# Kernel tuning notes

Measured on AMD Instinct MI355X. Metric: run time of the kernel, lower is better.

## Reference

```python
import jax, jax.numpy as jnp
import numpy as np

B, A, D, H = 2048, 32, 128, 256

def setup_inputs() -> dict:
    key = jax.random.key(0)
    ks = jax.random.split(key, 12)
    s = lambda fan_in: 1.0 / np.sqrt(fan_in)
    return {
        "obs": jax.random.normal(ks[0], (B, A, D), dtype=jnp.float32),
        "act": jax.random.normal(ks[1], (B, A, 8), dtype=jnp.float32),
        "enc_W": jax.random.uniform(ks[2], (H, D), jnp.float32, -s(D), s(D)),
        "enc_b": jax.random.uniform(ks[3], (H,), jnp.float32, -s(D), s(D)),
        "fobs_W": jax.random.uniform(ks[4], (H, H), jnp.float32, -s(H), s(H)),
        "fobs_b": jax.random.uniform(ks[5], (H,), jnp.float32, -s(H), s(H)),
        "W_ih": jax.random.uniform(ks[6], (3 * H, H), jnp.float32, -s(H), s(H)),
        "b_ih": jax.random.uniform(ks[7], (3 * H,), jnp.float32, -s(H), s(H)),
        "W_hh": jax.random.uniform(ks[8], (3 * H, H), jnp.float32, -s(H), s(H)),
        "b_hh": jax.random.uniform(ks[9], (3 * H,), jnp.float32, -s(H), s(H)),
        "dec_W": jax.random.uniform(ks[10], (1, H), jnp.float32, -s(H), s(H)),
        "dec_b": jax.random.uniform(ks[11], (1,), jnp.float32, -s(H), s(H)),
    }

def _gru_cell(x, h, W_ih, b_ih, W_hh, b_hh):
    # torch.nn.GRUCell: gates stacked as [reset, update, new]
    gi = x @ W_ih.T + b_ih          # [N, 3H]
    gh = h @ W_hh.T + b_hh          # [N, 3H]
    i_r, i_z, i_n = jnp.split(gi, 3, axis=-1)
    h_r, h_z, h_n = jnp.split(gh, 3, axis=-1)
    r = jax.nn.sigmoid(i_r + h_r)
    z = jax.nn.sigmoid(i_z + h_z)
    n = jnp.tanh(i_n + r * h_n)
    return (1.0 - z) * n + z * h

def reference(obs, act, enc_W, enc_b, fobs_W, fobs_b, W_ih, b_ih, W_hh, b_hh, dec_W, dec_b):
    b, a, d = obs.shape
    x = obs.reshape(b * a, d)                         # [B*A, D]
    e = jax.nn.relu(x @ enc_W.T + enc_b)              # encoder + ReLU
    h = e @ fobs_W.T + fobs_b                         # h_out
    # k = 0: comm input is zeros
    h = _gru_cell(jnp.zeros_like(h), h, W_ih, b_ih, W_hh, b_hh)
    # k = 1: masked mean over other agents == (sum_j h_j - h_i) / n_agents
    hA = h.reshape(b, a, -1)                          # [B, A, H]
    c = (hA.sum(axis=1, keepdims=True) - hA) / a      # [B, A, H]
    h = _gru_cell(c.reshape(b * a, -1), h, W_ih, b_ih, W_hh, b_hh)
    return (h @ dec_W.T + dec_b).reshape(b, a, -1)    # [B, A, 1]
```

## Files before the change

### kernel.cpp

```cpp
#include <hip/hip_runtime.h>
#include <hip/hip_fp16.h>


#define NB   2048
#define NA   32
#define DIN  128
#define HID  256
#define SA   264

typedef _Float16 half8  __attribute__((ext_vector_type(8)));
typedef float    float4v __attribute__((ext_vector_type(4)));

#define ENC_OFF    0
#define FOBS_OFF   32768
#define WIH_OFF    98304
#define WHH_OFF    294912
#define PREP_TOTAL 491520

__global__ void prep_weights(const float* __restrict__ encW, const float* __restrict__ fobsW,
                             const float* __restrict__ wih,  const float* __restrict__ whh,
                             _Float16* __restrict__ prep) {
    int F = blockIdx.x * 256 + threadIdx.x;
    if (F >= PREP_TOTAL) return;
    const float* src; int K, NT, local = F;
    if (F < FOBS_OFF)     { src = encW;  K = 128; NT = 16; }
    else if (F < WIH_OFF) { src = fobsW; K = 256; NT = 16; local = F - FOBS_OFF; }
    else if (F < WHH_OFF) { src = wih;   K = 256; NT = 48; local = F - WIH_OFF; }
    else                  { src = whh;   K = 256; NT = 48; local = F - WHH_OFF; }
    int j    = local & 7;
    int lane = (local >> 3) & 63;
    int t    = local >> 9;
    int nt   = t % NT;
    int ks   = t / NT;
    int col  = nt * 16 + (lane & 15);
    int k    = ks * 32 + ((lane >> 4) << 3) + j;
    prep[F] = (_Float16)src[col * K + k];
}

__device__ __forceinline__ float sigmoid_f(float x) {
    x = fminf(fmaxf(x, -30.f), 30.f);
    return 1.f / (1.f + __expf(-x));
}
__device__ __forceinline__ float tanh_f(float x) {
    x = fminf(fmaxf(x, -15.f), 15.f);
    float e = __expf(-2.f * x);
    return (1.f - e) / (1.f + e);
}

__device__ __forceinline__ void zero22(float4v a[2][2]) {
    float4v z = {0.f, 0.f, 0.f, 0.f};
    a[0][0] = z; a[0][1] = z; a[1][0] = z; a[1][1] = z;
}

template<int KSTEPS>
__device__ __forceinline__ void gemm_tile(const _Float16* __restrict__ Abuf,
        const _Float16* __restrict__ prepm, int NT, int ntg0,
        const float* __restrict__ raw, int K, int use_prep,
        int lane, float4v acc[2][2])
{
    const int l16 = lane & 15;
    const int kq  = (lane >> 4) << 3;
    #pragma unroll
    for (int ks = 0; ks < KSTEPS; ks++) {
        int kbase = ks * 32 + kq;
        half8 a0 = *(const half8*)(Abuf + l16 * SA + kbase);
        half8 a1 = *(const half8*)(Abuf + (16 + l16) * SA + kbase);
        half8 b0, b1;
        if (use_prep) {
            b0 = *(const half8*)(prepm + (((ks * NT + ntg0    ) * 64 + lane) << 3));
            b1 = *(const half8*)(prepm + (((ks * NT + ntg0 + 1) * 64 + lane) << 3));
        } else {
            #pragma unroll
            for (int j = 0; j < 8; j++) {
                b0[j] = (_Float16)raw[(ntg0 * 16 + l16) * K + kbase + j];
                b1[j] = (_Float16)raw[((ntg0 + 1) * 16 + l16) * K + kbase + j];
            }
        }
        acc[0][0] = __builtin_amdgcn_mfma_f32_16x16x32_f16(a0, b0, acc[0][0], 0, 0, 0);
        acc[0][1] = __builtin_amdgcn_mfma_f32_16x16x32_f16(a0, b1, acc[0][1], 0, 0, 0);
        acc[1][0] = __builtin_amdgcn_mfma_f32_16x16x32_f16(a1, b0, acc[1][0], 0, 0, 0);
        acc[1][1] = __builtin_amdgcn_mfma_f32_16x16x32_f16(a1, b1, acc[1][1], 0, 0, 0);
    }
}

__global__ __launch_bounds__(512) void commnet_fused(
    const float* __restrict__ obs, const _Float16* __restrict__ prep,
    const float* __restrict__ enc_b, const float* __restrict__ fobs_b,
    const float* __restrict__ b_ih, const float* __restrict__ b_hh,
    const float* __restrict__ dec_W, const float* __restrict__ dec_b,
    float* __restrict__ out,
    const float* __restrict__ encW, const float* __restrict__ fobsW,
    const float* __restrict__ wih, const float* __restrict__ whh,
    int use_prep)
{
    const int b    = blockIdx.x;
    const int tid  = threadIdx.x;
    const int lane = tid & 63;
    const int w    = tid >> 6;
    const int l16  = lane & 15;
    const int quad = lane >> 4;
    const int ntl0 = w * 2;

    __shared__ __align__(16) _Float16 sA[3][NA * SA];
    __shared__ float S[HID];

    const float* obsb = obs + (size_t)b * NA * DIN;
    for (int i = tid; i < NA * DIN; i += 512) {
        int r = i >> 7, k = i & 127;
        sA[0][r * SA + k] = (_Float16)obsb[i];
    }
    if (tid < HID) S[tid] = 0.f;
    __syncthreads();

    float4v acc[2][2];

    zero22(acc);
    gemm_tile<4>(&sA[0][0], prep + ENC_OFF, 16, ntl0, encW, DIN, use_prep, lane, acc);
    #pragma unroll
    for (int nn = 0; nn < 2; nn++) {
        int col = (ntl0 + nn) * 16 + l16;
        float bb = enc_b[col];
        #pragma unroll
        for (int mt = 0; mt < 2; mt++)
            #pragma unroll
            for (int r = 0; r < 4; r++) {
                int row = mt * 16 + quad * 4 + r;
                float v = acc[mt][nn][r] + bb;
                sA[1][row * SA + col] = (_Float16)fmaxf(v, 0.f);
            }
    }
    __syncthreads();

    zero22(acc);
    gemm_tile<8>(&sA[1][0], prep + FOBS_OFF, 16, ntl0, fobsW, HID, use_prep, lane, acc);
    #pragma unroll
    for (int nn = 0; nn < 2; nn++) {
        int col = (ntl0 + nn) * 16 + l16;
        float bb = fobs_b[col];
        #pragma unroll
        for (int mt = 0; mt < 2; mt++)
            #pragma unroll
            for (int r = 0; r < 4; r++) {
                int row = mt * 16 + quad * 4 + r;
                sA[0][row * SA + col] = (_Float16)(acc[mt][nn][r] + bb);
            }
    }
    __syncthreads();

    float rn[2][2][4];
    zero22(acc);
    gemm_tile<8>(&sA[0][0], prep + WHH_OFF, 48, 0 + ntl0, whh, HID, use_prep, lane, acc);
    #pragma unroll
    for (int nn = 0; nn < 2; nn++) {
        int col = (ntl0 + nn) * 16 + l16;
        float bi = b_ih[col], bh = b_hh[col];
        #pragma unroll
        for (int mt = 0; mt < 2; mt++)
            #pragma unroll
            for (int r = 0; r < 4; r++)
                rn[mt][nn][r] = sigmoid_f(bi + acc[mt][nn][r] + bh);
    }
    zero22(acc);
    gemm_tile<8>(&sA[0][0], prep + WHH_OFF, 48, 32 + ntl0, whh, HID, use_prep, lane, acc);
    #pragma unroll
    for (int nn = 0; nn < 2; nn++) {
        int col = (ntl0 + nn) * 16 + l16;
        float bi = b_ih[512 + col], bh = b_hh[512 + col];
        #pragma unroll
        for (int mt = 0; mt < 2; mt++)
            #pragma unroll
            for (int r = 0; r < 4; r++)
                rn[mt][nn][r] = tanh_f(bi + rn[mt][nn][r] * (acc[mt][nn][r] + bh));
    }
    zero22(acc);
    gemm_tile<8>(&sA[0][0], prep + WHH_OFF, 48, 16 + ntl0, whh, HID, use_prep, lane, acc);
    #pragma unroll
    for (int nn = 0; nn < 2; nn++) {
        int col = (ntl0 + nn) * 16 + l16;
        float bi = b_ih[256 + col], bh = b_hh[256 + col];
        float ssum = 0.f;
        #pragma unroll
        for (int mt = 0; mt < 2; mt++)
            #pragma unroll
            for (int r = 0; r < 4; r++) {
                int row = mt * 16 + quad * 4 + r;
                float z = sigmoid_f(bi + acc[mt][nn][r] + bh);
                float hold = (float)sA[0][row * SA + col];
                float h1 = (1.f - z) * rn[mt][nn][r] + z * hold;
                sA[1][row * SA + col] = (_Float16)h1;
                ssum += h1;
            }
        atomicAdd(&S[col], ssum);
    }
    __syncthreads();

    for (int i = tid; i < NA * HID; i += 512) {
        int r = i >> 8, k = i & 255;
        float hv = (float)sA[1][r * SA + k];
        sA[2][r * SA + k] = (_Float16)((S[k] - hv) * (1.f / 32.f));
    }
    __syncthreads();
    if (tid < NA) S[tid] = 0.f;
    __syncthreads();

    float4v acci[2][2], acch[2][2];
    zero22(acci); zero22(acch);
    gemm_tile<8>(&sA[2][0], prep + WIH_OFF, 48, 0 + ntl0, wih, HID, use_prep, lane, acci);
    gemm_tile<8>(&sA[1][0], prep + WHH_OFF, 48, 0 + ntl0, whh, HID, use_prep, lane, acch);
    #pragma unroll
    for (int nn = 0; nn < 2; nn++) {
        int col = (ntl0 + nn) * 16 + l16;
        float bi = b_ih[col], bh = b_hh[col];
        #pragma unroll
        for (int mt = 0; mt < 2; mt++)
            #pragma unroll
            for (int r = 0; r < 4; r++)
                rn[mt][nn][r] = sigmoid_f(acci[mt][nn][r] + bi + acch[mt][nn][r] + bh);
    }
    zero22(acci); zero22(acch);
    gemm_tile<8>(&sA[2][0], prep + WIH_OFF, 48, 32 + ntl0, wih, HID, use_prep, lane, acci);
    gemm_tile<8>(&sA[1][0], prep + WHH_OFF, 48, 32 + ntl0, whh, HID, use_prep, lane, acch);
    #pragma unroll
    for (int nn = 0; nn < 2; nn++) {
        int col = (ntl0 + nn) * 16 + l16;
        float bi = b_ih[512 + col], bh = b_hh[512 + col];
        #pragma unroll
        for (int mt = 0; mt < 2; mt++)
            #pragma unroll
            for (int r = 0; r < 4; r++)
                rn[mt][nn][r] = tanh_f((acci[mt][nn][r] + bi) + rn[mt][nn][r] * (acch[mt][nn][r] + bh));
    }
    zero22(acci); zero22(acch);
    gemm_tile<8>(&sA[2][0], prep + WIH_OFF, 48, 16 + ntl0, wih, HID, use_prep, lane, acci);
    gemm_tile<8>(&sA[1][0], prep + WHH_OFF, 48, 16 + ntl0, whh, HID, use_prep, lane, acch);
    #pragma unroll
    for (int nn = 0; nn < 2; nn++) {
        int col = (ntl0 + nn) * 16 + l16;
        float bi = b_ih[256 + col], bh = b_hh[256 + col];
        #pragma unroll
        for (int mt = 0; mt < 2; mt++)
            #pragma unroll
            for (int r = 0; r < 4; r++) {
                int row = mt * 16 + quad * 4 + r;
                float z = sigmoid_f(acci[mt][nn][r] + bi + acch[mt][nn][r] + bh);
                float h1v = (float)sA[1][row * SA + col];
                rn[mt][nn][r] = (1.f - z) * rn[mt][nn][r] + z * h1v;
            }
    }

    float dw0 = dec_W[(ntl0    ) * 16 + l16];
    float dw1 = dec_W[(ntl0 + 1) * 16 + l16];
    float p[2][4];
    #pragma unroll
    for (int mt = 0; mt < 2; mt++)
        #pragma unroll
        for (int r = 0; r < 4; r++)
            p[mt][r] = rn[mt][0][r] * dw0 + rn[mt][1][r] * dw1;
    #pragma unroll
    for (int m = 1; m <= 8; m <<= 1) {
        #pragma unroll
        for (int mt = 0; mt < 2; mt++)
            #pragma unroll
            for (int r = 0; r < 4; r++)
                p[mt][r] += __shfl_xor(p[mt][r], m);
    }
    if (l16 == 0) {
        #pragma unroll
        for (int mt = 0; mt < 2; mt++)
            #pragma unroll
            for (int r = 0; r < 4; r++)
                atomicAdd(&S[mt * 16 + quad * 4 + r], p[mt][r]);
    }
    __syncthreads();
    if (tid < NA) out[(size_t)b * NA + tid] = S[tid] + dec_b[0];
}

extern "C" void kernel_launch(void* const* d_in, const int* in_sizes, int n_in,
                              void* d_out, int out_size, void* d_ws, size_t ws_size,
                              hipStream_t stream) {
    const float* obs   = (const float*)d_in[0];
    const float* encW  = (const float*)d_in[2];
    const float* encb  = (const float*)d_in[3];
    const float* fobsW = (const float*)d_in[4];
    const float* fobsb = (const float*)d_in[5];
    const float* wih   = (const float*)d_in[6];
    const float* bih   = (const float*)d_in[7];
    const float* whh   = (const float*)d_in[8];
    const float* bhh   = (const float*)d_in[9];
    const float* decW  = (const float*)d_in[10];
    const float* decb  = (const float*)d_in[11];
    float* out = (float*)d_out;

    _Float16* prep = (_Float16*)d_ws;
    int use_prep = (ws_size >= (size_t)PREP_TOTAL * sizeof(_Float16)) ? 1 : 0;
    if (use_prep) {
        prep_weights<<<(PREP_TOTAL + 255) / 256, 256, 0, stream>>>(encW, fobsW, wih, whh, prep);
    }
    commnet_fused<<<NB, 512, 0, stream>>>(obs, prep, encb, fobsb, bih, bhh, decW, decb, out,
                                          encW, fobsW, wih, whh, use_prep);
}
```

Baseline: 289.6 us.

## Widen per-wave tiles to 4 N-tiles, halve block size, shrink LDS footprint

The fused kernel now runs 256 threads per block, and each wave computes a 32x64 output tile with 8 accumulators, so each A fragment loaded from LDS feeds four MFMAs. The comm input overwrites the first h buffer, which drops LDS from three 32x264 half buffers to two and lets more blocks fit per CU. The second GRU step reuses one accumulator set for the ih and hh products of the r/z gates, and the decoder dot product is folded into the final gate loop. The weight-prep kernel and the obs/comm staging loops are vectorized, at the cost of higher register pressure from the larger accumulator tile.

```diff
diff --git a/kernel.cpp b/kernel.cpp
--- a/kernel.cpp
+++ b/kernel.cpp
@@ -9,6 +9,7 @@
 #define SA   264
 
 typedef _Float16 half8  __attribute__((ext_vector_type(8)));
+typedef _Float16 half4_t __attribute__((ext_vector_type(4)));
 typedef float    float4v __attribute__((ext_vector_type(4)));
 
 #define ENC_OFF    0
@@ -17,24 +18,26 @@
 #define WHH_OFF    294912
 #define PREP_TOTAL 491520
 
-__global__ void prep_weights(const float* __restrict__ encW, const float* __restrict__ fobsW,
-                             const float* __restrict__ wih,  const float* __restrict__ whh,
-                             _Float16* __restrict__ prep) {
-    int F = blockIdx.x * 256 + threadIdx.x;
-    if (F >= PREP_TOTAL) return;
-    const float* src; int K, NT, local = F;
-    if (F < FOBS_OFF)     { src = encW;  K = 128; NT = 16; }
-    else if (F < WIH_OFF) { src = fobsW; K = 256; NT = 16; local = F - FOBS_OFF; }
-    else if (F < WHH_OFF) { src = wih;   K = 256; NT = 48; local = F - WIH_OFF; }
-    else                  { src = whh;   K = 256; NT = 48; local = F - WHH_OFF; }
-    int j    = local & 7;
-    int lane = (local >> 3) & 63;
-    int t    = local >> 9;
-    int nt   = t % NT;
-    int ks   = t / NT;
-    int col  = nt * 16 + (lane & 15);
-    int k    = ks * 32 + ((lane >> 4) << 3) + j;
-    prep[F] = (_Float16)src[col * K + k];
+__global__ __launch_bounds__(256) void prep_weights(
+        const float* __restrict__ encW, const float* __restrict__ fobsW,
+        const float* __restrict__ wih,  const float* __restrict__ whh,
+        _Float16* __restrict__ prep) {
+    int W = blockIdx.x * 4 + (threadIdx.x >> 6);
+    int lane = threadIdx.x & 63;
+    const float* src; int K, NT, base, idx;
+    if (W < 64)       { src = encW;  K = 128; NT = 16; base = ENC_OFF;  idx = W; }
+    else if (W < 192) { src = fobsW; K = 256; NT = 16; base = FOBS_OFF; idx = W - 64; }
+    else if (W < 576) { src = wih;   K = 256; NT = 48; base = WIH_OFF;  idx = W - 192; }
+    else              { src = whh;   K = 256; NT = 48; base = WHH_OFF;  idx = W - 576; }
+    int nt = idx % NT, ks = idx / NT;
+    int l16 = lane & 15, q = lane >> 4;
+    const float* s = src + (size_t)(nt * 16 + l16) * K + ks * 32 + q * 8;
+    float4v f0 = *(const float4v*)s;
+    float4v f1 = *(const float4v*)(s + 4);
+    half8 h;
+    h[0] = (_Float16)f0[0]; h[1] = (_Float16)f0[1]; h[2] = (_Float16)f0[2]; h[3] = (_Float16)f0[3];
+    h[4] = (_Float16)f1[0]; h[5] = (_Float16)f1[1]; h[6] = (_Float16)f1[2]; h[7] = (_Float16)f1[3];
+    *(half8*)(prep + base + (((size_t)(ks * NT + nt) * 64 + lane) << 3)) = h;
 }
 
 __device__ __forceinline__ float sigmoid_f(float x) {
@@ -47,16 +50,19 @@
     return (1.f - e) / (1.f + e);
 }
 
-__device__ __forceinline__ void zero22(float4v a[2][2]) {
+__device__ __forceinline__ void zero24(float4v a[2][4]) {
     float4v z = {0.f, 0.f, 0.f, 0.f};
-    a[0][0] = z; a[0][1] = z; a[1][0] = z; a[1][1] = z;
+    #pragma unroll
+    for (int m = 0; m < 2; m++)
+        #pragma unroll
+        for (int n = 0; n < 4; n++) a[m][n] = z;
 }
 
 template<int KSTEPS>
-__device__ __forceinline__ void gemm_tile(const _Float16* __restrict__ Abuf,
+__device__ __forceinline__ void gemm_tile4(const _Float16* __restrict__ Abuf,
         const _Float16* __restrict__ prepm, int NT, int ntg0,
         const float* __restrict__ raw, int K, int use_prep,
-        int lane, float4v acc[2][2])
+        int lane, float4v acc[2][4])
 {
     const int l16 = lane & 15;
     const int kq  = (lane >> 4) << 3;
@@ -65,25 +71,23 @@
         int kbase = ks * 32 + kq;
         half8 a0 = *(const half8*)(Abuf + l16 * SA + kbase);
         half8 a1 = *(const half8*)(Abuf + (16 + l16) * SA + kbase);
-        half8 b0, b1;
-        if (use_prep) {
-            b0 = *(const half8*)(prepm + (((ks * NT + ntg0    ) * 64 + lane) << 3));
-            b1 = *(const half8*)(prepm + (((ks * NT + ntg0 + 1) * 64 + lane) << 3));
-        } else {
-            #pragma unroll
-            for (int j = 0; j < 8; j++) {
-                b0[j] = (_Float16)raw[(ntg0 * 16 + l16) * K + kbase + j];
-                b1[j] = (_Float16)raw[((ntg0 + 1) * 16 + l16) * K + kbase + j];
-            }
+        #pragma unroll
+        for (int nn = 0; nn < 4; nn++) {
+            half8 b;
+            if (use_prep) {
+                b = *(const half8*)(prepm + (((ks * NT + ntg0 + nn) * 64 + lane) << 3));
+            } else {
+                #pragma unroll
+                for (int j = 0; j < 8; j++)
+                    b[j] = (_Float16)raw[((ntg0 + nn) * 16 + l16) * K + kbase + j];
+            }
+            acc[0][nn] = __builtin_amdgcn_mfma_f32_16x16x32_f16(a0, b, acc[0][nn], 0, 0, 0);
+            acc[1][nn] = __builtin_amdgcn_mfma_f32_16x16x32_f16(a1, b, acc[1][nn], 0, 0, 0);
         }
-        acc[0][0] = __builtin_amdgcn_mfma_f32_16x16x32_f16(a0, b0, acc[0][0], 0, 0, 0);
-        acc[0][1] = __builtin_amdgcn_mfma_f32_16x16x32_f16(a0, b1, acc[0][1], 0, 0, 0);
-        acc[1][0] = __builtin_amdgcn_mfma_f32_16x16x32_f16(a1, b0, acc[1][0], 0, 0, 0);
-        acc[1][1] = __builtin_amdgcn_mfma_f32_16x16x32_f16(a1, b1, acc[1][1], 0, 0, 0);
-    }
-}
-
-__global__ __launch_bounds__(512) void commnet_fused(
+    }
+}
+
+__global__ __launch_bounds__(256, 4) void commnet_fused(
     const float* __restrict__ obs, const _Float16* __restrict__ prep,
     const float* __restrict__ enc_b, const float* __restrict__ fobs_b,
     const float* __restrict__ b_ih, const float* __restrict__ b_hh,
@@ -99,25 +103,34 @@
     const int w    = tid >> 6;
     const int l16  = lane & 15;
     const int quad = lane >> 4;
-    const int ntl0 = w * 2;
-
-    __shared__ __align__(16) _Float16 sA[3][NA * SA];
+    const int ntl0 = w * 4;
+
+    __shared__ __align__(16) _Float16 sA[2][NA * SA];
     __shared__ float S[HID];
+    __shared__ float D[NA];
 
     const float* obsb = obs + (size_t)b * NA * DIN;
-    for (int i = tid; i < NA * DIN; i += 512) {
-        int r = i >> 7, k = i & 127;
-        sA[0][r * SA + k] = (_Float16)obsb[i];
+    #pragma unroll
+    for (int j = 0; j < 4; j++) {
+        int i = tid + j * 256;
+        float4v v = ((const float4v*)obsb)[i];
+        int r = i >> 5, kd = (i & 31) * 4;
+        half4_t hv;
+        hv[0] = (_Float16)v[0]; hv[1] = (_Float16)v[1];
+        hv[2] = (_Float16)v[2]; hv[3] = (_Float16)v[3];
+        *(half4_t*)(&sA[0][r * SA + kd]) = hv;
     }
     if (tid < HID) S[tid] = 0.f;
-    __syncthreads();
-
-    float4v acc[2][2];
-
-    zero22(acc);
-    gemm_tile<4>(&sA[0][0], prep + ENC_OFF, 16, ntl0, encW, DIN, use_prep, lane, acc);
-    #pragma unroll
-    for (int nn = 0; nn < 2; nn++) {
+    if (tid < NA)  D[tid] = 0.f;
+    __syncthreads();
+
+    float4v acc[2][4];
+    float rn[2][4][4];
+
+    zero24(acc);
+    gemm_tile4<4>(&sA[0][0], prep + ENC_OFF, 16, ntl0, encW, DIN, use_prep, lane, acc);
+    #pragma unroll
+    for (int nn = 0; nn < 4; nn++) {
         int col = (ntl0 + nn) * 16 + l16;
         float bb = enc_b[col];
         #pragma unroll
@@ -125,16 +138,15 @@
             #pragma unroll
             for (int r = 0; r < 4; r++) {
                 int row = mt * 16 + quad * 4 + r;
-                float v = acc[mt][nn][r] + bb;
-                sA[1][row * SA + col] = (_Float16)fmaxf(v, 0.f);
-            }
-    }
-    __syncthreads();
-
-    zero22(acc);
-    gemm_tile<8>(&sA[1][0], prep + FOBS_OFF, 16, ntl0, fobsW, HID, use_prep, lane, acc);
-    #pragma unroll
-    for (int nn = 0; nn < 2; nn++) {
+                sA[1][row * SA + col] = (_Float16)fmaxf(acc[mt][nn][r] + bb, 0.f);
+            }
+    }
+    __syncthreads();
+
+    zero24(acc);
+    gemm_tile4<8>(&sA[1][0], prep + FOBS_OFF, 16, ntl0, fobsW, HID, use_prep, lane, acc);
+    #pragma unroll
+    for (int nn = 0; nn < 4; nn++) {
         int col = (ntl0 + nn) * 16 + l16;
         float bb = fobs_b[col];
         #pragma unroll
@@ -147,11 +159,10 @@
     }
     __syncthreads();
 
-    float rn[2][2][4];
-    zero22(acc);
-    gemm_tile<8>(&sA[0][0], prep + WHH_OFF, 48, 0 + ntl0, whh, HID, use_prep, lane, acc);
-    #pragma unroll
-    for (int nn = 0; nn < 2; nn++) {
+    zero24(acc);
+    gemm_tile4<8>(&sA[0][0], prep + WHH_OFF, 48, 0 + ntl0, whh, HID, use_prep, lane, acc);
+    #pragma unroll
+    for (int nn = 0; nn < 4; nn++) {
         int col = (ntl0 + nn) * 16 + l16;
         float bi = b_ih[col], bh = b_hh[col];
         #pragma unroll
@@ -160,10 +171,10 @@
             for (int r = 0; r < 4; r++)
                 rn[mt][nn][r] = sigmoid_f(bi + acc[mt][nn][r] + bh);
     }
-    zero22(acc);
-    gemm_tile<8>(&sA[0][0], prep + WHH_OFF, 48, 32 + ntl0, whh, HID, use_prep, lane, acc);
-    #pragma unroll
-    for (int nn = 0; nn < 2; nn++) {
+    zero24(acc);
+    gemm_tile4<8>(&sA[0][0], prep + WHH_OFF, 48, 32 + ntl0, whh, HID, use_prep, lane, acc);
+    #pragma unroll
+    for (int nn = 0; nn < 4; nn++) {
         int col = (ntl0 + nn) * 16 + l16;
         float bi = b_ih[512 + col], bh = b_hh[512 + col];
         #pragma unroll
@@ -172,10 +183,10 @@
             for (int r = 0; r < 4; r++)
                 rn[mt][nn][r] = tanh_f(bi + rn[mt][nn][r] * (acc[mt][nn][r] + bh));
     }
-    zero22(acc);
-    gemm_tile<8>(&sA[0][0], prep + WHH_OFF, 48, 16 + ntl0, whh, HID, use_prep, lane, acc);
-    #pragma unroll
-    for (int nn = 0; nn < 2; nn++) {
+    zero24(acc);
+    gemm_tile4<8>(&sA[0][0], prep + WHH_OFF, 48, 16 + ntl0, whh, HID, use_prep, lane, acc);
+    #pragma unroll
+    for (int nn = 0; nn < 4; nn++) {
         int col = (ntl0 + nn) * 16 + l16;
         float bi = b_ih[256 + col], bh = b_hh[256 + col];
         float ssum = 0.f;
@@ -194,85 +205,95 @@
     }
     __syncthreads();
 
-    for (int i = tid; i < NA * HID; i += 512) {
-        int r = i >> 8, k = i & 255;
-        float hv = (float)sA[1][r * SA + k];
-        sA[2][r * SA + k] = (_Float16)((S[k] - hv) * (1.f / 32.f));
-    }
-    __syncthreads();
-    if (tid < NA) S[tid] = 0.f;
-    __syncthreads();
-
-    float4v acci[2][2], acch[2][2];
-    zero22(acci); zero22(acch);
-    gemm_tile<8>(&sA[2][0], prep + WIH_OFF, 48, 0 + ntl0, wih, HID, use_prep, lane, acci);
-    gemm_tile<8>(&sA[1][0], prep + WHH_OFF, 48, 0 + ntl0, whh, HID, use_prep, lane, acch);
-    #pragma unroll
-    for (int nn = 0; nn < 2; nn++) {
-        int col = (ntl0 + nn) * 16 + l16;
-        float bi = b_ih[col], bh = b_hh[col];
-        #pragma unroll
-        for (int mt = 0; mt < 2; mt++)
-            #pragma unroll
-            for (int r = 0; r < 4; r++)
-                rn[mt][nn][r] = sigmoid_f(acci[mt][nn][r] + bi + acch[mt][nn][r] + bh);
-    }
-    zero22(acci); zero22(acch);
-    gemm_tile<8>(&sA[2][0], prep + WIH_OFF, 48, 32 + ntl0, wih, HID, use_prep, lane, acci);
-    gemm_tile<8>(&sA[1][0], prep + WHH_OFF, 48, 32 + ntl0, whh, HID, use_prep, lane, acch);
-    #pragma unroll
-    for (int nn = 0; nn < 2; nn++) {
-        int col = (ntl0 + nn) * 16 + l16;
-        float bi = b_ih[512 + col], bh = b_hh[512 + col];
-        #pragma unroll
-        for (int mt = 0; mt < 2; mt++)
-            #pragma unroll
-            for (int r = 0; r < 4; r++)
-                rn[mt][nn][r] = tanh_f((acci[mt][nn][r] + bi) + rn[mt][nn][r] * (acch[mt][nn][r] + bh));
-    }
-    zero22(acci); zero22(acch);
-    gemm_tile<8>(&sA[2][0], prep + WIH_OFF, 48, 16 + ntl0, wih, HID, use_prep, lane, acci);
-    gemm_tile<8>(&sA[1][0], prep + WHH_OFF, 48, 16 + ntl0, whh, HID, use_prep, lane, acch);
-    #pragma unroll
-    for (int nn = 0; nn < 2; nn++) {
-        int col = (ntl0 + nn) * 16 + l16;
-        float bi = b_ih[256 + col], bh = b_hh[256 + col];
+    #pragma unroll
+    for (int j = 0; j < 8; j++) {
+        int i = tid + j * 256;
+        int r = i >> 6, cg = (i & 63) * 4;
+        half4_t hv = *(const half4_t*)(&sA[1][r * SA + cg]);
+        half4_t cv;
+        #pragma unroll
+        for (int t = 0; t < 4; t++)
+            cv[t] = (_Float16)((S[cg + t] - (float)hv[t]) * (1.f / 32.f));
+        *(half4_t*)(&sA[0][r * SA + cg]) = cv;
+    }
+    __syncthreads();
+
+    zero24(acc);
+    gemm_tile4<8>(&sA[0][0], prep + WIH_OFF, 48, 0 + ntl0, wih, HID, use_prep, lane, acc);
+    gemm_tile4<8>(&sA[1][0], prep + WHH_OFF, 48, 0 + ntl0, whh, HID, use_prep, lane, acc);
+    #pragma unroll
+    for (int nn = 0; nn < 4; nn++) {
+        int col = (ntl0 + nn) * 16 + l16;
+        float bb = b_ih[col] + b_hh[col];
+        #pragma unroll
+        for (int mt = 0; mt < 2; mt++)
+            #pragma unroll
+            for (int r = 0; r < 4; r++)
+                rn[mt][nn][r] = sigmoid_f(acc[mt][nn][r] + bb);
+    }
+    zero24(acc);
+    gemm_tile4<8>(&sA[1][0], prep + WHH_OFF, 48, 32 + ntl0, whh, HID, use_prep, lane, acc);
+    #pragma unroll
+    for (int nn = 0; nn < 4; nn++) {
+        int col = (ntl0 + nn) * 16 + l16;
+        float bh = b_hh[512 + col];
+        #pragma unroll
+        for (int mt = 0; mt < 2; mt++)
+            #pragma unroll
+            for (int r = 0; r < 4; r++)
+                rn[mt][nn][r] = rn[mt][nn][r] * (acc[mt][nn][r] + bh);
+    }
+    zero24(acc);
+    gemm_tile4<8>(&sA[0][0], prep + WIH_OFF, 48, 32 + ntl0, wih, HID, use_prep, lane, acc);
+    #pragma unroll
+    for (int nn = 0; nn < 4; nn++) {
+        int col = (ntl0 + nn) * 16 + l16;
+        float bi = b_ih[512 + col];
+        #pragma unroll
+        for (int mt = 0; mt < 2; mt++)
+            #pragma unroll
+            for (int r = 0; r < 4; r++)
+                rn[mt][nn][r] = tanh_f(acc[mt][nn][r] + bi + rn[mt][nn][r]);
+    }
+    zero24(acc);
+    gemm_tile4<8>(&sA[0][0], prep + WIH_OFF, 48, 16 + ntl0, wih, HID, use_prep, lane, acc);
+    gemm_tile4<8>(&sA[1][0], prep + WHH_OFF, 48, 16 + ntl0, whh, HID, use_prep, lane, acc);
+    float dw[4];
+    #pragma unroll
+    for (int nn = 0; nn < 4; nn++) dw[nn] = dec_W[(ntl0 + nn) * 16 + l16];
+    float p[2][4] = {};
+    #pragma unroll
+    for (int nn = 0; nn < 4; nn++) {
+        int col = (ntl0 + nn) * 16 + l16;
+        float bb = b_ih[256 + col] + b_hh[256 + col];
         #pragma unroll
         for (int mt = 0; mt < 2; mt++)
             #pragma unroll
             for (int r = 0; r < 4; r++) {
                 int row = mt * 16 + quad * 4 + r;
-                float z = sigmoid_f(acci[mt][nn][r] + bi + acch[mt][nn][r] + bh);
+                float z = sigmoid_f(acc[mt][nn][r] + bb);
                 float h1v = (float)sA[1][row * SA + col];
-                rn[mt][nn][r] = (1.f - z) * rn[mt][nn][r] + z * h1v;
-            }
-    }
-
-    float dw0 = dec_W[(ntl0    ) * 16 + l16];
-    float dw1 = dec_W[(ntl0 + 1) * 16 + l16];
-    float p[2][4];
-    #pragma unroll
-    for (int mt = 0; mt < 2; mt++)
-        #pragma unroll
-        for (int r = 0; r < 4; r++)
-            p[mt][r] = rn[mt][0][r] * dw0 + rn[mt][1][r] * dw1;
-    #pragma unroll
-    for (int m = 1; m <= 8; m <<= 1) {
+                float h2 = (1.f - z) * rn[mt][nn][r] + z * h1v;
+                p[mt][r] += h2 * dw[nn];
+            }
+    }
+
+    #pragma unroll
+    for (int m = 1; m <= 8; m <<= 1)
         #pragma unroll
         for (int mt = 0; mt < 2; mt++)
             #pragma unroll
             for (int r = 0; r < 4; r++)
                 p[mt][r] += __shfl_xor(p[mt][r], m);
-    }
     if (l16 == 0) {
         #pragma unroll
         for (int mt = 0; mt < 2; mt++)
             #pragma unroll
             for (int r = 0; r < 4; r++)
-                atomicAdd(&S[mt * 16 + quad * 4 + r], p[mt][r]);
-    }
-    __syncthreads();
-    if (tid < NA) out[(size_t)b * NA + tid] = S[tid] + dec_b[0];
+                atomicAdd(&D[mt * 16 + quad * 4 + r], p[mt][r]);
+    }
+    __syncthreads();
+    if (tid < NA) out[(size_t)b * NA + tid] = D[tid] + dec_b[0];
 }
 
 extern "C" void kernel_launch(void* const* d_in, const int* in_sizes, int n_in,
@@ -294,8 +315,8 @@
     _Float16* prep = (_Float16*)d_ws;
     int use_prep = (ws_size >= (size_t)PREP_TOTAL * sizeof(_Float16)) ? 1 : 0;
     if (use_prep) {
-        prep_weights<<<(PREP_TOTAL + 255) / 256, 256, 0, stream>>>(encW, fobsW, wih, whh, prep);
-    }
-    commnet_fused<<<NB, 512, 0, stream>>>(obs, prep, encb, fobsb, bih, bhh, decW, decb, out,
+        prep_weights<<<240, 256, 0, stream>>>(encW, fobsW, wih, whh, prep);
+    }
+    commnet_fused<<<NB, 256, 0, stream>>>(obs, prep, encb, fobsb, bih, bhh, decW, decb, out,
                                           encW, fobsW, wih, whh, use_prep);
 }
```

Measured after the change: 446.8 us. +54.3%, slower.
